# Performance work log

Hardware: AMD Instinct MI355X
Metric: run time of the kernel (lower is better)

## Reference

```python
import jax, jax.numpy as jnp
import numpy as np

EPS = 1e-5
H = W = 14  # spatial grid, N = H*W = 196


def layernorm(x, g, b):
    m = x.mean(-1, keepdims=True)
    v = ((x - m) ** 2).mean(-1, keepdims=True)
    return (x - m) * jax.lax.rsqrt(v + EPS) * g + b


def fem_step(x, s):
    # x: [B, C, H, W]; blockwise instance-norm -> sigmoid gate -> 0.5*x + 0.5*attn*x
    B, C, h, w = x.shape
    nbh = -(-h // s)
    nbw = -(-w // s)
    idh = np.arange(h) // s
    idw = np.arange(w) // s
    bid_np = (idh[:, None] * nbw + idw[None, :]).reshape(-1)  # [h*w]
    cnt = jnp.asarray(np.bincount(bid_np, minlength=nbh * nbw).astype(np.float32))
    bid = jnp.asarray(bid_np)
    xt = x.reshape(B, C, h * w).transpose(2, 0, 1)  # [HW, B, C]
    s1 = jax.ops.segment_sum(xt, bid, num_segments=nbh * nbw)      # [nblk, B, C]
    s2 = jax.ops.segment_sum(xt * xt, bid, num_segments=nbh * nbw)
    mean = s1 / cnt[:, None, None]
    var = s2 / cnt[:, None, None] - mean * mean  # biased var, as F.instance_norm
    attn = jax.nn.sigmoid((xt - mean[bid]) * jax.lax.rsqrt(var[bid] + EPS))
    out = 0.5 * xt * (1.0 + attn)  # 0.5*x + 0.5*attn*x
    return out.transpose(1, 2, 0).reshape(B, C, h, w)


def fem(x):
    # p=[2,1,0] -> block sizes H//4=3, H//2=7, H//1=14
    for s in (H // 4, H // 2, H):
        x = fem_step(x, s)
    return x


def setup_inputs() -> dict:
    key = jax.random.key(0)
    ks = jax.random.split(key, 4)
    B, N, C = 64, H * W, 1024
    hid = 4 * C
    return {
        "x": jax.random.normal(ks[0], (B, N, C), jnp.float32),
        "ln1_g": jnp.ones((C,), jnp.float32),
        "ln1_b": jnp.zeros((C,), jnp.float32),
        "cw": jax.random.normal(ks[1], (H, W // 2 + 1, C, 2), jnp.float32) * 0.02,
        "ln2_g": jnp.ones((C,), jnp.float32),
        "ln2_b": jnp.zeros((C,), jnp.float32),
        "fc1_w": jax.random.normal(ks[2], (C, hid), jnp.float32) * 0.02,
        "fc1_b": jnp.zeros((hid,), jnp.float32),
        "fc2_w": jax.random.normal(ks[3], (hid, C), jnp.float32) * 0.02,
        "fc2_b": jnp.zeros((C,), jnp.float32),
    }


def reference(x, ln1_g, ln1_b, cw, ln2_g, ln2_b, fc1_w, fc1_b, fc2_w, fc2_b):
    B, N, C = x.shape
    # FFT global filter
    y = layernorm(x, ln1_g, ln1_b)
    yf = jnp.fft.rfft2(y.reshape(B, H, W, C), axes=(1, 2), norm="ortho")
    yf = yf * (cw[..., 0] + 1j * cw[..., 1])
    y = jnp.fft.irfft2(yf, s=(H, W), axes=(1, 2), norm="ortho").reshape(B, N, C)
    # MLP
    y = layernorm(y, ln2_g, ln2_b)
    y = jax.nn.gelu(y @ fc1_w + fc1_b, approximate=False) @ fc2_w + fc2_b
    # FEM on [B, C, H, W]
    y = fem(y.transpose(0, 2, 1).reshape(B, C, H, W))
    y = y.reshape(B, C, N).transpose(0, 2, 1)
    return x + y
```

## Files before the change

kernel.cpp:

```cpp
#include <hip/hip_runtime.h>

constexpr int CB = 64;
constexpr int CHH = 14, CWW = 14;
constexpr int CN = 196;
constexpr int CC = 1024;
constexpr int CROWS = CB * CN;
constexpr int CKW = 8;

constexpr float C14[14] = {
  1.0f, 0.9009688679024191f, 0.6234898018587336f, 0.2225209339563144f,
  -0.2225209339563144f, -0.6234898018587336f, -0.9009688679024191f, -1.0f,
  -0.9009688679024191f, -0.6234898018587336f, -0.2225209339563144f,
  0.2225209339563144f, 0.6234898018587336f, 0.9009688679024191f };
constexpr float S14[14] = {
  0.0f, 0.4338837391175581f, 0.7818314824680298f, 0.9749279121818236f,
  0.9749279121818236f, 0.7818314824680298f, 0.4338837391175581f, 0.0f,
  -0.4338837391175581f, -0.7818314824680298f, -0.9749279121818236f,
  -0.9749279121818236f, -0.7818314824680298f, -0.4338837391175581f };

typedef __attribute__((ext_vector_type(8))) short bf16x8;
typedef __attribute__((ext_vector_type(4))) float f32x4;

__device__ __forceinline__ unsigned short f2bf(float f) {
  unsigned u = __builtin_bit_cast(unsigned, f);
  u += 0x7FFFu + ((u >> 16) & 1u);
  return (unsigned short)(u >> 16);
}
__device__ __forceinline__ float bf2f(unsigned short h) {
  return __builtin_bit_cast(float, (unsigned)h << 16);
}
__device__ __forceinline__ unsigned pack2(float re, float im) {
  return (unsigned)f2bf(re) | ((unsigned)f2bf(im) << 16);
}

__device__ __forceinline__ void gload_lds16(const void* g, void* l) {
  __builtin_amdgcn_global_load_lds(
      (const __attribute__((address_space(1))) void*)g,
      (__attribute__((address_space(3))) void*)l, 16, 0, 0);
}

#define WAITV(N)  asm volatile("s_waitcnt vmcnt(" #N ")" ::: "memory")

template<int INBF>
__global__ __launch_bounds__(256)
void ln_kernel(const void* __restrict__ in_, const float* __restrict__ gam,
               const float* __restrict__ bet, unsigned short* __restrict__ outb)
{
  const int row = blockIdx.x;
  const int t = threadIdx.x;
  float4 v;
  if (INBF) {
    const ushort4 u = ((const ushort4*)in_)[(size_t)row * 256 + t];
    v = make_float4(bf2f(u.x), bf2f(u.y), bf2f(u.z), bf2f(u.w));
  } else {
    v = ((const float4*)in_)[(size_t)row * 256 + t];
  }
  float s  = v.x + v.y + v.z + v.w;
  float s2 = v.x*v.x + v.y*v.y + v.z*v.z + v.w*v.w;
  #pragma unroll
  for (int o = 32; o > 0; o >>= 1) { s += __shfl_down(s, o); s2 += __shfl_down(s2, o); }
  __shared__ float red[8];
  const int wid = t >> 6, lane = t & 63;
  if (lane == 0) { red[wid] = s; red[4 + wid] = s2; }
  __syncthreads();
  s  = red[0] + red[1] + red[2] + red[3];
  s2 = red[4] + red[5] + red[6] + red[7];
  const float mean = s * (1.0f / CC);
  const float var  = s2 * (1.0f / CC) - mean * mean;
  const float r = rsqrtf(var + 1e-5f);
  const float4 g4 = *(const float4*)(gam + t * 4);
  const float4 b4 = *(const float4*)(bet + t * 4);
  ushort4 p;
  p.x = f2bf((v.x - mean) * r * g4.x + b4.x);
  p.y = f2bf((v.y - mean) * r * g4.y + b4.y);
  p.z = f2bf((v.z - mean) * r * g4.z + b4.z);
  p.w = f2bf((v.w - mean) * r * g4.w + b4.w);
  *(ushort4*)(outb + (size_t)row * CC + t * 4) = p;
}

__global__ __launch_bounds__(256)
void fft_w_fwd(const unsigned short* __restrict__ y, unsigned* __restrict__ Az)
{
  const int t = threadIdx.x;
  const int bid = blockIdx.x;
  const int h = bid % 14;
  const int b = bid / 14;
  const int c4 = t * 4;
  const size_t base = ((size_t)b * CN + (size_t)h * CWW) * CC + c4;
  float v[14][4];
  #pragma unroll
  for (int w = 0; w < 14; w++) {
    const ushort4 u = *(const ushort4*)(y + base + (size_t)w * CC);
    v[w][0] = bf2f(u.x); v[w][1] = bf2f(u.y); v[w][2] = bf2f(u.z); v[w][3] = bf2f(u.w);
  }
  const size_t obase = (((size_t)b * CHH + h) * CKW) * CC + c4;
  #pragma unroll
  for (int kw = 0; kw < 8; kw++) {
    float sr[4] = {}, si[4] = {};
    #pragma unroll
    for (int w = 0; w < 14; w++) {
      const int m = (w * kw) % 14;
      #pragma unroll
      for (int j = 0; j < 4; j++) {
        sr[j] += v[w][j] * C14[m];
        si[j] -= v[w][j] * S14[m];
      }
    }
    uint4 o;
    o.x = pack2(sr[0], si[0]); o.y = pack2(sr[1], si[1]);
    o.z = pack2(sr[2], si[2]); o.w = pack2(sr[3], si[3]);
    *(uint4*)(Az + obase + (size_t)kw * CC) = o;
  }
}

__global__ __launch_bounds__(256)
void fft_h_filt(const unsigned* __restrict__ Az, const float* __restrict__ cw,
                unsigned* __restrict__ Bz)
{
  const int t = threadIdx.x;
  const int bid = blockIdx.x;
  const int half = bid & 1;
  const int tmp = bid >> 1;
  const int kw = tmp & 7;
  const int b = tmp >> 3;
  const int c2 = half * 512 + t * 2;
  const size_t base = (((size_t)b * CHH) * CKW + kw) * CC + c2;
  float ar[14][2], ai[14][2];
  #pragma unroll
  for (int h = 0; h < 14; h++) {
    const uint2 u = *(const uint2*)(Az + base + (size_t)h * (CKW * CC));
    ar[h][0] = bf2f((unsigned short)(u.x & 0xffff)); ai[h][0] = bf2f((unsigned short)(u.x >> 16));
    ar[h][1] = bf2f((unsigned short)(u.y & 0xffff)); ai[h][1] = bf2f((unsigned short)(u.y >> 16));
  }
  float fr[14][2], fi[14][2];
  #pragma unroll
  for (int kh = 0; kh < 14; kh++) {
    float yr[2] = {}, yi[2] = {};
    #pragma unroll
    for (int h = 0; h < 14; h++) {
      const int m = (h * kh) % 14;
      #pragma unroll
      for (int j = 0; j < 2; j++) {
        yr[j] += ar[h][j] * C14[m] + ai[h][j] * S14[m];
        yi[j] += ai[h][j] * C14[m] - ar[h][j] * S14[m];
      }
    }
    const float4 w4 = *(const float4*)(cw + ((size_t)(kh * CKW + kw) * CC + c2) * 2);
    fr[kh][0] = yr[0] * w4.x - yi[0] * w4.y; fi[kh][0] = yr[0] * w4.y + yi[0] * w4.x;
    fr[kh][1] = yr[1] * w4.z - yi[1] * w4.w; fi[kh][1] = yr[1] * w4.w + yi[1] * w4.z;
  }
  #pragma unroll
  for (int h = 0; h < 14; h++) {
    float sr[2] = {}, si[2] = {};
    #pragma unroll
    for (int kh = 0; kh < 14; kh++) {
      const int m = (h * kh) % 14;
      #pragma unroll
      for (int j = 0; j < 2; j++) {
        sr[j] += fr[kh][j] * C14[m] - fi[kh][j] * S14[m];
        si[j] += fr[kh][j] * S14[m] + fi[kh][j] * C14[m];
      }
    }
    uint2 o;
    o.x = pack2(sr[0], si[0]); o.y = pack2(sr[1], si[1]);
    *(uint2*)(Bz + base + (size_t)h * (CKW * CC)) = o;
  }
}

__global__ __launch_bounds__(256)
void fft_w_inv(const unsigned* __restrict__ Bz, unsigned short* __restrict__ y2)
{
  const int t = threadIdx.x;
  const int bid = blockIdx.x;
  const int h = bid % 14;
  const int b = bid / 14;
  const int c4 = t * 4;
  const size_t ibase = (((size_t)b * CHH + h) * CKW) * CC + c4;
  float br[8][4], bi[8][4];
  #pragma unroll
  for (int k = 0; k < 8; k++) {
    const uint4 u = *(const uint4*)(Bz + ibase + (size_t)k * CC);
    br[k][0] = bf2f((unsigned short)(u.x & 0xffff)); bi[k][0] = bf2f((unsigned short)(u.x >> 16));
    br[k][1] = bf2f((unsigned short)(u.y & 0xffff)); bi[k][1] = bf2f((unsigned short)(u.y >> 16));
    br[k][2] = bf2f((unsigned short)(u.z & 0xffff)); bi[k][2] = bf2f((unsigned short)(u.z >> 16));
    br[k][3] = bf2f((unsigned short)(u.w & 0xffff)); bi[k][3] = bf2f((unsigned short)(u.w >> 16));
  }
  const size_t obase = ((size_t)b * CN + (size_t)h * CWW) * CC + c4;
  #pragma unroll
  for (int w = 0; w < 14; w++) {
    float s[4];
    #pragma unroll
    for (int j = 0; j < 4; j++)
      s[j] = br[0][j] + ((w & 1) ? -br[7][j] : br[7][j]);
    #pragma unroll
    for (int k = 1; k < 7; k++) {
      const int m = (w * k) % 14;
      #pragma unroll
      for (int j = 0; j < 4; j++)
        s[j] += 2.0f * (br[k][j] * C14[m] - bi[k][j] * S14[m]);
    }
    ushort4 o;
    o.x = f2bf(s[0] * (1.0f / 196.0f)); o.y = f2bf(s[1] * (1.0f / 196.0f));
    o.z = f2bf(s[2] * (1.0f / 196.0f)); o.w = f2bf(s[3] * (1.0f / 196.0f));
    *(ushort4*)(y2 + obase + (size_t)w * CC) = o;
  }
}

__global__ __launch_bounds__(256)
void transpose_f32_bf16(const float* __restrict__ in, unsigned short* __restrict__ out,
                        int R, int Ccols)
{
  __shared__ float tile[32][33];
  const int tx = threadIdx.x & 31;
  const int ty = threadIdx.x >> 5;
  const int cb = blockIdx.x * 32;
  const int rb = blockIdx.y * 32;
  #pragma unroll
  for (int i = 0; i < 32; i += 8)
    tile[ty + i][tx] = in[(size_t)(rb + ty + i) * Ccols + cb + tx];
  __syncthreads();
  #pragma unroll
  for (int i = 0; i < 32; i += 8)
    out[(size_t)(cb + ty + i) * R + rb + tx] = f2bf(tile[tx][ty + i]);
}

template<int DO_GELU>
__global__ __launch_bounds__(256, 4)
void gemm128(const unsigned short* __restrict__ A, const unsigned short* __restrict__ BT,
             const float* __restrict__ bias, unsigned short* __restrict__ C,
             int M, int N, int K)
{
  __shared__ __align__(16) char sA[16384];
  __shared__ __align__(16) char sB[16384];
  const int t = threadIdx.x;
  const int wid = t >> 6, lane = t & 63;
  const int wm = wid >> 1, wn = wid & 1;
  const int lrow = lane & 15, qk = lane >> 4;
  const int dq = qk << 4;

  const int nbx = N >> 7, nby = M >> 7;
  const int per = nbx << 3;
  const int fullg = nby >> 3;
  int by, bx;
  if ((int)blockIdx.x < fullg * per) {
    const int g = blockIdx.x / per, r = blockIdx.x % per;
    by = (g << 3) + (r & 7); bx = r >> 3;
  } else {
    const int r = blockIdx.x - fullg * per;
    const int rem = nby - (fullg << 3);
    by = (fullg << 3) + r % rem; bx = r / rem;
  }
  const int brow = by << 7, bcol = bx << 7;

  const int vr = t >> 3;
  const int cl = ((t ^ (t >> 3)) & 7) << 3;
  const int dstb = t * 16;

  f32x4 acc[4][4] = {};

  for (int k0 = 0; k0 < K; k0 += 64) {
    __syncthreads();
    #pragma unroll
    for (int i = 0; i < 4; ++i) {
      gload_lds16(A  + (size_t)(brow + i * 32 + vr) * K + k0 + cl, sA + i * 4096 + dstb);
      gload_lds16(BT + (size_t)(bcol + i * 32 + vr) * K + k0 + cl, sB + i * 4096 + dstb);
    }
    WAITV(0);
    __syncthreads();
    #pragma unroll
    for (int ks = 0; ks < 2; ++ks) {
      bf16x8 af[4], bf[4];
      #pragma unroll
      for (int mf = 0; mf < 4; ++mf) {
        const int row = wm * 64 + mf * 16 + lrow;
        af[mf] = *(const bf16x8*)(sA + row * 128 + (((ks << 6) | dq) ^ ((row & 7) << 4)));
      }
      #pragma unroll
      for (int nf = 0; nf < 4; ++nf) {
        const int row = wn * 64 + nf * 16 + lrow;
        bf[nf] = *(const bf16x8*)(sB + row * 128 + (((ks << 6) | dq) ^ ((row & 7) << 4)));
      }
      #pragma unroll
      for (int mf = 0; mf < 4; ++mf)
        #pragma unroll
        for (int nf = 0; nf < 4; ++nf)
          acc[mf][nf] = __builtin_amdgcn_mfma_f32_16x16x32_bf16(af[mf], bf[nf],
                                                                acc[mf][nf], 0, 0, 0);
    }
  }

  #pragma unroll
  for (int mf = 0; mf < 4; ++mf) {
    #pragma unroll
    for (int nf = 0; nf < 4; ++nf) {
      const int ccol = bcol + wn * 64 + nf * 16 + lrow;
      const float bb = bias[ccol];
      #pragma unroll
      for (int j = 0; j < 4; ++j) {
        const int r = brow + wm * 64 + mf * 16 + qk * 4 + j;
        float v = acc[mf][nf][j] + bb;
        if (DO_GELU) v = 0.5f * v * (1.0f + erff(v * 0.70710678118654752f));
        C[(size_t)r * N + ccol] = f2bf(v);
      }
    }
  }
}

__device__ __forceinline__ void fem_block(unsigned short* col, int t,
                                          int h0, int nh, int w0, int nw)
{
  float s = 0.f, s2 = 0.f;
  for (int ih = 0; ih < nh; ih++)
    for (int iw = 0; iw < nw; iw++) {
      const float v = bf2f(col[((h0 + ih) * 14 + w0 + iw) * 128 + t]);
      s += v; s2 += v * v;
    }
  const float inv = 1.0f / (float)(nh * nw);
  const float m = s * inv;
  const float var = s2 * inv - m * m;
  const float r = rsqrtf(var + 1e-5f);
  for (int ih = 0; ih < nh; ih++)
    for (int iw = 0; iw < nw; iw++) {
      const int idx = ((h0 + ih) * 14 + w0 + iw) * 128 + t;
      const float v = bf2f(col[idx]);
      const float a = 1.0f / (1.0f + __expf(-(v - m) * r));
      col[idx] = f2bf(0.5f * v * (1.0f + a));
    }
}

__global__ __launch_bounds__(128)
void fem_kernel(const unsigned short* __restrict__ z, const float* __restrict__ x,
                float* __restrict__ out)
{
  __shared__ unsigned short buf[CN * 128];
  const int t = threadIdx.x;
  const int b = blockIdx.x >> 3;
  const int cc = blockIdx.x & 7;
  const int c = cc * 128 + t;
  const size_t base = (size_t)b * CN * CC + c;
  #pragma unroll 4
  for (int n = 0; n < CN; n++) buf[n * 128 + t] = z[base + (size_t)n * CC];
  const int st3[5] = {0, 3, 6, 9, 12};
  const int ln3[5] = {3, 3, 3, 3, 2};
  for (int i = 0; i < 5; i++)
    for (int j = 0; j < 5; j++)
      fem_block(buf, t, st3[i], ln3[i], st3[j], ln3[j]);
  for (int i = 0; i < 2; i++)
    for (int j = 0; j < 2; j++)
      fem_block(buf, t, i * 7, 7, j * 7, 7);
  fem_block(buf, t, 0, 14, 0, 14);
  #pragma unroll 4
  for (int n = 0; n < CN; n++)
    out[base + (size_t)n * CC] = x[base + (size_t)n * CC] + bf2f(buf[n * 128 + t]);
}

extern "C" void kernel_launch(void* const* d_in, const int* in_sizes, int n_in,
                              void* d_out, int out_size, void* d_ws, size_t ws_size,
                              hipStream_t stream) {
  const float* x     = (const float*)d_in[0];
  const float* ln1_g = (const float*)d_in[1];
  const float* ln1_b = (const float*)d_in[2];
  const float* cw    = (const float*)d_in[3];
  const float* ln2_g = (const float*)d_in[4];
  const float* ln2_b = (const float*)d_in[5];
  const float* fc1_w = (const float*)d_in[6];
  const float* fc1_b = (const float*)d_in[7];
  const float* fc2_w = (const float*)d_in[8];
  const float* fc2_b = (const float*)d_in[9];
  float* out = (float*)d_out;
  char* ws = (char*)d_ws;

  const size_t SZ = (size_t)CB * CHH * CKW * CC * 4;
  unsigned* Az = (unsigned*)(ws);
  unsigned* Bz = (unsigned*)(ws + SZ);
  unsigned short* A1   = (unsigned short*)(ws);
  unsigned short* W1T  = (unsigned short*)(ws + SZ);
  unsigned short* W2T  = (unsigned short*)(ws + SZ + (size_t)4096 * 1024 * 2);
  unsigned short* Hmid = (unsigned short*)(ws + SZ + (size_t)4096 * 1024 * 4);
  unsigned short* Z    = (unsigned short*)(ws);
  unsigned short* y12  = (unsigned short*)d_out;

  ln_kernel<0><<<CROWS, 256, 0, stream>>>(x, ln1_g, ln1_b, y12);
  fft_w_fwd<<<CB * CHH, 256, 0, stream>>>(y12, Az);
  fft_h_filt<<<CB * CKW * 2, 256, 0, stream>>>(Az, cw, Bz);
  fft_w_inv<<<CB * CHH, 256, 0, stream>>>(Bz, y12);
  ln_kernel<1><<<CROWS, 256, 0, stream>>>(y12, ln2_g, ln2_b, A1);
  transpose_f32_bf16<<<dim3(4096 / 32, 1024 / 32), 256, 0, stream>>>(fc1_w, W1T, 1024, 4096);
  transpose_f32_bf16<<<dim3(1024 / 32, 4096 / 32), 256, 0, stream>>>(fc2_w, W2T, 4096, 1024);
  gemm128<1><<<dim3(3136), 256, 0, stream>>>(A1, W1T, fc1_b, Hmid, CROWS, 4096, 1024);
  gemm128<0><<<dim3(784), 256, 0, stream>>>(Hmid, W2T, fc2_b, Z, CROWS, 1024, 4096);
  fem_kernel<<<CB * 8, 128, 0, stream>>>(Z, x, out);
}
```

Measured before the change: 459.3 us.

## Fuse layernorms into the width-FFT forward and inverse kernels

```diff
diff --git a/kernel.cpp b/kernel.cpp
--- a/kernel.cpp
+++ b/kernel.cpp
@@ -41,45 +41,9 @@
 
 #define WAITV(N)  asm volatile("s_waitcnt vmcnt(" #N ")" ::: "memory")
 
-template<int INBF>
 __global__ __launch_bounds__(256)
-void ln_kernel(const void* __restrict__ in_, const float* __restrict__ gam,
-               const float* __restrict__ bet, unsigned short* __restrict__ outb)
-{
-  const int row = blockIdx.x;
-  const int t = threadIdx.x;
-  float4 v;
-  if (INBF) {
-    const ushort4 u = ((const ushort4*)in_)[(size_t)row * 256 + t];
-    v = make_float4(bf2f(u.x), bf2f(u.y), bf2f(u.z), bf2f(u.w));
-  } else {
-    v = ((const float4*)in_)[(size_t)row * 256 + t];
-  }
-  float s  = v.x + v.y + v.z + v.w;
-  float s2 = v.x*v.x + v.y*v.y + v.z*v.z + v.w*v.w;
-  #pragma unroll
-  for (int o = 32; o > 0; o >>= 1) { s += __shfl_down(s, o); s2 += __shfl_down(s2, o); }
-  __shared__ float red[8];
-  const int wid = t >> 6, lane = t & 63;
-  if (lane == 0) { red[wid] = s; red[4 + wid] = s2; }
-  __syncthreads();
-  s  = red[0] + red[1] + red[2] + red[3];
-  s2 = red[4] + red[5] + red[6] + red[7];
-  const float mean = s * (1.0f / CC);
-  const float var  = s2 * (1.0f / CC) - mean * mean;
-  const float r = rsqrtf(var + 1e-5f);
-  const float4 g4 = *(const float4*)(gam + t * 4);
-  const float4 b4 = *(const float4*)(bet + t * 4);
-  ushort4 p;
-  p.x = f2bf((v.x - mean) * r * g4.x + b4.x);
-  p.y = f2bf((v.y - mean) * r * g4.y + b4.y);
-  p.z = f2bf((v.z - mean) * r * g4.z + b4.z);
-  p.w = f2bf((v.w - mean) * r * g4.w + b4.w);
-  *(ushort4*)(outb + (size_t)row * CC + t * 4) = p;
-}
-
-__global__ __launch_bounds__(256)
-void fft_w_fwd(const unsigned short* __restrict__ y, unsigned* __restrict__ Az)
+void ln_fftw(const float* __restrict__ x, const float* __restrict__ gam,
+             const float* __restrict__ bet, unsigned* __restrict__ Az)
 {
   const int t = threadIdx.x;
   const int bid = blockIdx.x;
@@ -88,10 +52,38 @@
   const int c4 = t * 4;
   const size_t base = ((size_t)b * CN + (size_t)h * CWW) * CC + c4;
   float v[14][4];
-  #pragma unroll
-  for (int w = 0; w < 14; w++) {
-    const ushort4 u = *(const ushort4*)(y + base + (size_t)w * CC);
-    v[w][0] = bf2f(u.x); v[w][1] = bf2f(u.y); v[w][2] = bf2f(u.z); v[w][3] = bf2f(u.w);
+  float sw[14], qw[14];
+  #pragma unroll
+  for (int w = 0; w < 14; w++) {
+    const float4 u = *(const float4*)(x + base + (size_t)w * CC);
+    v[w][0] = u.x; v[w][1] = u.y; v[w][2] = u.z; v[w][3] = u.w;
+    sw[w] = u.x + u.y + u.z + u.w;
+    qw[w] = u.x*u.x + u.y*u.y + u.z*u.z + u.w*u.w;
+  }
+  __shared__ float redS[14][4], redQ[14][4];
+  const int wid = t >> 6, lane = t & 63;
+  #pragma unroll
+  for (int w = 0; w < 14; w++) {
+    float a = sw[w], q = qw[w];
+    #pragma unroll
+    for (int o = 32; o > 0; o >>= 1) { a += __shfl_down(a, o); q += __shfl_down(q, o); }
+    if (lane == 0) { redS[w][wid] = a; redQ[w][wid] = q; }
+  }
+  __syncthreads();
+  const float4 g4 = *(const float4*)(gam + c4);
+  const float4 b4 = *(const float4*)(bet + c4);
+  const float gg[4] = {g4.x, g4.y, g4.z, g4.w};
+  const float bb[4] = {b4.x, b4.y, b4.z, b4.w};
+  #pragma unroll
+  for (int w = 0; w < 14; w++) {
+    const float a = redS[w][0] + redS[w][1] + redS[w][2] + redS[w][3];
+    const float q = redQ[w][0] + redQ[w][1] + redQ[w][2] + redQ[w][3];
+    const float mean = a * (1.0f / CC);
+    const float var  = q * (1.0f / CC) - mean * mean;
+    const float r = rsqrtf(var + 1e-5f);
+    #pragma unroll
+    for (int j = 0; j < 4; j++)
+      v[w][j] = (v[w][j] - mean) * r * gg[j] + bb[j];
   }
   const size_t obase = (((size_t)b * CHH + h) * CKW) * CC + c4;
   #pragma unroll
@@ -168,7 +160,8 @@
 }
 
 __global__ __launch_bounds__(256)
-void fft_w_inv(const unsigned* __restrict__ Bz, unsigned short* __restrict__ y2)
+void fftinv_ln(const unsigned* __restrict__ Bz, const float* __restrict__ gam,
+               const float* __restrict__ bet, unsigned short* __restrict__ A1)
 {
   const int t = threadIdx.x;
   const int bid = blockIdx.x;
@@ -185,7 +178,8 @@
     br[k][2] = bf2f((unsigned short)(u.z & 0xffff)); bi[k][2] = bf2f((unsigned short)(u.z >> 16));
     br[k][3] = bf2f((unsigned short)(u.w & 0xffff)); bi[k][3] = bf2f((unsigned short)(u.w >> 16));
   }
-  const size_t obase = ((size_t)b * CN + (size_t)h * CWW) * CC + c4;
+  float y[14][4];
+  float sw[14], qw[14];
   #pragma unroll
   for (int w = 0; w < 14; w++) {
     float s[4];
@@ -199,10 +193,42 @@
       for (int j = 0; j < 4; j++)
         s[j] += 2.0f * (br[k][j] * C14[m] - bi[k][j] * S14[m]);
     }
+    float a = 0.f, q = 0.f;
+    #pragma unroll
+    for (int j = 0; j < 4; j++) {
+      y[w][j] = s[j] * (1.0f / 196.0f);
+      a += y[w][j];
+      q += y[w][j] * y[w][j];
+    }
+    sw[w] = a; qw[w] = q;
+  }
+  __shared__ float redS[14][4], redQ[14][4];
+  const int wid = t >> 6, lane = t & 63;
+  #pragma unroll
+  for (int w = 0; w < 14; w++) {
+    float a = sw[w], q = qw[w];
+    #pragma unroll
+    for (int o = 32; o > 0; o >>= 1) { a += __shfl_down(a, o); q += __shfl_down(q, o); }
+    if (lane == 0) { redS[w][wid] = a; redQ[w][wid] = q; }
+  }
+  __syncthreads();
+  const float4 g4 = *(const float4*)(gam + c4);
+  const float4 b4 = *(const float4*)(bet + c4);
+  const float gg[4] = {g4.x, g4.y, g4.z, g4.w};
+  const float bb[4] = {b4.x, b4.y, b4.z, b4.w};
+  #pragma unroll
+  for (int w = 0; w < 14; w++) {
+    const float a = redS[w][0] + redS[w][1] + redS[w][2] + redS[w][3];
+    const float q = redQ[w][0] + redQ[w][1] + redQ[w][2] + redQ[w][3];
+    const float mean = a * (1.0f / CC);
+    const float var  = q * (1.0f / CC) - mean * mean;
+    const float r = rsqrtf(var + 1e-5f);
     ushort4 o;
-    o.x = f2bf(s[0] * (1.0f / 196.0f)); o.y = f2bf(s[1] * (1.0f / 196.0f));
-    o.z = f2bf(s[2] * (1.0f / 196.0f)); o.w = f2bf(s[3] * (1.0f / 196.0f));
-    *(ushort4*)(y2 + obase + (size_t)w * CC) = o;
+    o.x = f2bf((y[w][0] - mean) * r * gg[0] + bb[0]);
+    o.y = f2bf((y[w][1] - mean) * r * gg[1] + bb[1]);
+    o.z = f2bf((y[w][2] - mean) * r * gg[2] + bb[2]);
+    o.w = f2bf((y[w][3] - mean) * r * gg[3] + bb[3]);
+    *(ushort4*)(A1 + ((size_t)b * CN + (size_t)h * CWW + w) * CC + c4) = o;
   }
 }
 
@@ -378,13 +404,10 @@
   unsigned short* W2T  = (unsigned short*)(ws + SZ + (size_t)4096 * 1024 * 2);
   unsigned short* Hmid = (unsigned short*)(ws + SZ + (size_t)4096 * 1024 * 4);
   unsigned short* Z    = (unsigned short*)(ws);
-  unsigned short* y12  = (unsigned short*)d_out;
-
-  ln_kernel<0><<<CROWS, 256, 0, stream>>>(x, ln1_g, ln1_b, y12);
-  fft_w_fwd<<<CB * CHH, 256, 0, stream>>>(y12, Az);
+
+  ln_fftw<<<CB * CHH, 256, 0, stream>>>(x, ln1_g, ln1_b, Az);
   fft_h_filt<<<CB * CKW * 2, 256, 0, stream>>>(Az, cw, Bz);
-  fft_w_inv<<<CB * CHH, 256, 0, stream>>>(Bz, y12);
-  ln_kernel<1><<<CROWS, 256, 0, stream>>>(y12, ln2_g, ln2_b, A1);
+  fftinv_ln<<<CB * CHH, 256, 0, stream>>>(Bz, ln2_g, ln2_b, A1);
   transpose_f32_bf16<<<dim3(4096 / 32, 1024 / 32), 256, 0, stream>>>(fc1_w, W1T, 1024, 4096);
   transpose_f32_bf16<<<dim3(1024 / 32, 4096 / 32), 256, 0, stream>>>(fc2_w, W2T, 4096, 1024);
   gemm128<1><<<dim3(3136), 256, 0, stream>>>(A1, W1T, fc1_b, Hmid, CROWS, 4096, 1024);
```

New measurement: 456.2 us. No clear change (-0.7%).
